# Kernel tuning notes

Hardware: AMD Instinct MI355X
Metric: run time of the kernel (lower is better)

The kernel has to match this reference:

```python
import jax, jax.numpy as jnp
import numpy as np

B, S, D_MODEL = 2, 2048, 1024
NUM_HEADS, ATTN_DIM = 16, 64


def setup_inputs() -> dict:
    key = jax.random.key(0)
    ks = jax.random.split(key, 9)
    scale = 1.0 / np.sqrt(D_MODEL)
    states = jax.random.normal(ks[0], (B, S, D_MODEL), dtype=jnp.float32)
    Wq = jax.random.normal(ks[1], (D_MODEL, NUM_HEADS * ATTN_DIM), dtype=jnp.float32) * scale
    bq = jnp.zeros((NUM_HEADS * ATTN_DIM,), dtype=jnp.float32)
    Wk = jax.random.normal(ks[2], (D_MODEL, NUM_HEADS * ATTN_DIM), dtype=jnp.float32) * scale
    bk = jnp.zeros((NUM_HEADS * ATTN_DIM,), dtype=jnp.float32)
    Wv = jax.random.normal(ks[3], (D_MODEL, NUM_HEADS * ATTN_DIM), dtype=jnp.float32) * scale
    bv = jnp.zeros((NUM_HEADS * ATTN_DIM,), dtype=jnp.float32)
    Wo = jax.random.normal(ks[4], (NUM_HEADS * ATTN_DIM, D_MODEL), dtype=jnp.float32) * scale
    bo = jnp.zeros((D_MODEL,), dtype=jnp.float32)
    return {"states": states, "Wq": Wq, "bq": bq, "Wk": Wk, "bk": bk,
            "Wv": Wv, "bv": bv, "Wo": Wo, "bo": bo}


def reference(states, Wq, bq, Wk, bk, Wv, bv, Wo, bo):
    b, s, _ = states.shape
    h, d = NUM_HEADS, ATTN_DIM

    def proj(W, bias):
        # tanh-activated Dense, then split heads: [b, s, h*d] -> [b, h, s, d]
        y = jnp.tanh(states @ W + bias)
        return y.reshape(b, s, h, d).transpose(0, 2, 1, 3)

    q, k, v = proj(Wq, bq), proj(Wk, bk), proj(Wv, bv)
    # scores: [b, h, s, s]
    alpha = jnp.einsum("bhqd,bhkd->bhqk", q, k) / jnp.sqrt(jnp.float32(d))
    # causal mask (row i attends to cols 0..i); masked logits set to float32.min
    causal = jnp.tril(jnp.ones((s, s), dtype=bool))
    alpha = jnp.where(causal, alpha, jnp.finfo(jnp.float32).min)
    alpha = jax.nn.softmax(alpha, axis=-1)
    ctx = jnp.einsum("bhqk,bhkd->bhqd", alpha, v)  # [b, h, s, d]
    ctx = ctx.transpose(0, 2, 1, 3).reshape(b, s, h * d)
    return jnp.tanh(ctx @ Wo + bo)
```

## Files before the change

### kernel.cpp

```cpp
#include <hip/hip_runtime.h>
#include <math.h>

typedef unsigned short u16;
typedef __attribute__((ext_vector_type(4))) float f32x4;
typedef __attribute__((ext_vector_type(16))) float f32x16;
typedef __attribute__((ext_vector_type(8))) short bf16x8;

#define B_ 2
#define S_ 2048
#define DM 1024
#define H_ 16
#define AD 64
#define ME 4194304
#define SC 0.18033688011112042f
#define SMAX 12.0f

#define GLL(g, s) __builtin_amdgcn_global_load_lds( \
  (const __attribute__((address_space(1))) void*)(g), \
  (__attribute__((address_space(3))) void*)(s), 16, 0, 0)

__device__ inline u16 f2bf(float f) {
  union { float f; unsigned u; } v; v.f = f;
  unsigned r = v.u + 0x7fffu + ((v.u >> 16) & 1u);
  return (u16)(r >> 16);
}

__device__ inline unsigned cvt_pk_bf16(float lo, float hi) {
  unsigned r;
  asm("v_cvt_pk_bf16_f32 %0, %1, %2" : "=v"(r) : "v"(lo), "v"(hi));
  return r;
}

__device__ inline float fast_tanh(float x) {
  float e = __builtin_amdgcn_exp2f(x * 2.885390081777927f);
  return 1.f - 2.f * __builtin_amdgcn_rcpf(e + 1.f);
}

__global__ __launch_bounds__(256) void conv_states(const float* __restrict__ in,
                                                   u16* __restrict__ out) {
  int i = (blockIdx.x * 256 + threadIdx.x) * 8;
  const float4* p = (const float4*)(in + i);
  float4 a = p[0], b = p[1];
  bf16x8 o;
  o[0] = (short)f2bf(a.x); o[1] = (short)f2bf(a.y);
  o[2] = (short)f2bf(a.z); o[3] = (short)f2bf(a.w);
  o[4] = (short)f2bf(b.x); o[5] = (short)f2bf(b.y);
  o[6] = (short)f2bf(b.z); o[7] = (short)f2bf(b.w);
  *(bf16x8*)&out[i] = o;
}

__global__ void transpose_w(const float* __restrict__ Wq, const float* __restrict__ Wk,
                            const float* __restrict__ Wv, const float* __restrict__ Wo,
                            u16* __restrict__ Wt) {
  __shared__ float t[32][33];
  int z = blockIdx.z;
  const float* W = (z == 0) ? Wq : (z == 1) ? Wk : (z == 2) ? Wv : Wo;
  u16* out = Wt + (size_t)z * DM * DM;
  int n0 = blockIdx.x * 32, k0 = blockIdx.y * 32;
  int tx = threadIdx.x, ty = threadIdx.y;
  t[ty][tx] = W[(k0 + ty) * DM + n0 + tx];
  __syncthreads();
  out[(n0 + ty) * DM + k0 + tx] = f2bf(t[tx][ty]);
}

__global__ __launch_bounds__(256) void qkv_gemm(
    const u16* __restrict__ A, const u16* __restrict__ Wt,
    const float* __restrict__ bq, const float* __restrict__ bk, const float* __restrict__ bv,
    u16* __restrict__ Qw, u16* __restrict__ Kw, u16* __restrict__ Vtw) {
  __shared__ __attribute__((aligned(16))) u16 lA[128 * 32];
  __shared__ __attribute__((aligned(16))) u16 lB[128 * 32];
  const int z = blockIdx.z;
  const u16* Bt = Wt + (size_t)z * DM * DM;
  const int lin = blockIdx.y * 8 + blockIdx.x;
  const int tile = (lin & 7) * 32 + (lin >> 3);
  const int m0 = (tile >> 3) * 128, n0 = (tile & 7) * 128;
  const int tid = threadIdx.x;
  const int wid = tid >> 6, l = tid & 63;
  const int lr = l & 15, lk = l >> 4;
  const int wm = (wid >> 1) * 64, wn = (wid & 1) * 64;
  const int srow = wid * 32 + (l >> 2);
  const int scol = (l & 3) * 8;

  f32x4 acc[4][4] = {};

  for (int k0 = 0; k0 < DM; k0 += 32) {
    const u16* gA = &A[(size_t)(m0 + srow) * DM + k0 + scol];
    const u16* gB = &Bt[(size_t)(n0 + srow) * DM + k0 + scol];
    GLL(gA,           lA + wid * 1024);
    GLL(gA + 16 * DM, lA + wid * 1024 + 512);
    GLL(gB,           lB + wid * 1024);
    GLL(gB + 16 * DM, lB + wid * 1024 + 512);
    __syncthreads();
    bf16x8 af[4], bfr[4];
#pragma unroll
    for (int g = 0; g < 4; ++g) {
      af[g]  = *(const bf16x8*)&lA[(wm + g * 16 + lr) * 32 + lk * 8];
      bfr[g] = *(const bf16x8*)&lB[(wn + g * 16 + lr) * 32 + lk * 8];
    }
#pragma unroll
    for (int mg = 0; mg < 4; ++mg)
#pragma unroll
      for (int ng = 0; ng < 4; ++ng)
        acc[mg][ng] = __builtin_amdgcn_mfma_f32_16x16x32_bf16(af[mg], bfr[ng], acc[mg][ng], 0, 0, 0);
    __syncthreads();
  }

  const float* bias = (z == 0) ? bq : (z == 1) ? bk : bv;
#pragma unroll
  for (int mg = 0; mg < 4; ++mg)
#pragma unroll
    for (int ng = 0; ng < 4; ++ng)
#pragma unroll
      for (int r = 0; r < 4; ++r) {
        int m = m0 + wm + mg * 16 + lk * 4 + r;
        int n = n0 + wn + ng * 16 + lr;
        float v = fast_tanh(acc[mg][ng][r] + bias[n]);
        if (z == 0) v *= SC;
        u16 h16 = f2bf(v);
        int bb = m >> 11, s = m & 2047, hh = n >> 6, d = n & 63;
        if (z == 2) Vtw[((size_t)(bb * H_ + hh) * AD + d) * S_ + s] = h16;
        else ((z == 0) ? Qw : Kw)[((size_t)(bb * H_ + hh) * S_ + s) * AD + d] = h16;
      }
}

__global__ __launch_bounds__(256) void out_gemm(
    const u16* __restrict__ A, const u16* __restrict__ Bt,
    const float* __restrict__ bo, float* __restrict__ out) {
  __shared__ __attribute__((aligned(16))) u16 lA[128 * 32];
  __shared__ __attribute__((aligned(16))) u16 lB[128 * 32];
  const int lin = blockIdx.y * 8 + blockIdx.x;
  const int tile = (lin & 7) * 32 + (lin >> 3);
  const int m0 = (tile >> 3) * 128, n0 = (tile & 7) * 128;
  const int tid = threadIdx.x;
  const int wid = tid >> 6, l = tid & 63;
  const int lr = l & 15, lk = l >> 4;
  const int wm = (wid >> 1) * 64, wn = (wid & 1) * 64;
  const int srow = wid * 32 + (l >> 2);
  const int scol = (l & 3) * 8;

  f32x4 acc[4][4] = {};

  for (int k0 = 0; k0 < DM; k0 += 32) {
    const u16* gA = &A[(size_t)(m0 + srow) * DM + k0 + scol];
    const u16* gB = &Bt[(size_t)(n0 + srow) * DM + k0 + scol];
    GLL(gA,           lA + wid * 1024);
    GLL(gA + 16 * DM, lA + wid * 1024 + 512);
    GLL(gB,           lB + wid * 1024);
    GLL(gB + 16 * DM, lB + wid * 1024 + 512);
    __syncthreads();
    bf16x8 af[4], bfr[4];
#pragma unroll
    for (int g = 0; g < 4; ++g) {
      af[g]  = *(const bf16x8*)&lA[(wm + g * 16 + lr) * 32 + lk * 8];
      bfr[g] = *(const bf16x8*)&lB[(wn + g * 16 + lr) * 32 + lk * 8];
    }
#pragma unroll
    for (int mg = 0; mg < 4; ++mg)
#pragma unroll
      for (int ng = 0; ng < 4; ++ng)
        acc[mg][ng] = __builtin_amdgcn_mfma_f32_16x16x32_bf16(af[mg], bfr[ng], acc[mg][ng], 0, 0, 0);
    __syncthreads();
  }

#pragma unroll
  for (int mg = 0; mg < 4; ++mg)
#pragma unroll
    for (int ng = 0; ng < 4; ++ng)
#pragma unroll
      for (int r = 0; r < 4; ++r) {
        int m = m0 + wm + mg * 16 + lk * 4 + r;
        int n = n0 + wn + ng * 16 + lr;
        out[(size_t)m * DM + n] = fast_tanh(acc[mg][ng][r] + bo[n]);
      }
}

__global__ __launch_bounds__(256, 3) void attn_kernel(
    const u16* __restrict__ Q, const u16* __restrict__ K,
    const u16* __restrict__ Vt, u16* __restrict__ ctx,
    float* __restrict__ O0, float* __restrict__ O1, float* __restrict__ O2,
    float* __restrict__ L0, float* __restrict__ L1, float* __restrict__ L2) {
  __shared__ __attribute__((aligned(16))) char smem[32768];
  const int u = blockIdx.x >> 5;
  const int bh = blockIdx.x & 31;
  int t, lo;
  if (u < 11)       { t = u + 5;  lo = 0; }
  else if (u < 16)  { t = u;      lo = 6; }
  else if (u == 16) { t = 4;      lo = 0; }
  else if (u == 17) { t = 10;     lo = 6; }
  else { int r = u - 18, g = r / 3, c = r % 3;
         if (c == 0)      { t = 3 - g;  lo = 0; }
         else if (c == 1) { t = 9 - g;  lo = 6; }
         else             { t = 15 - g; lo = 12; } }
  const int hi = (lo == 0) ? (t < 5 ? t : 5) : ((lo == 6) ? (t < 11 ? t : 11) : t);

  const int tid = threadIdx.x, wl = tid >> 6, l = tid & 63;
  const int lq = l & 31, hl = l >> 5;
  const int q0 = t * 128 + wl * 32;

  const char* Qb = (const char*)(Q + (size_t)bh * S_ * AD);
  const char* Kb = (const char*)(K + (size_t)bh * S_ * AD);
  const char* Vb = (const char*)(Vt + (size_t)bh * AD * S_);

  int kcst[4], vcst[4], ldso[4];
#pragma unroll
  for (int i = 0; i < 4; ++i) {
    int c = wl * 4 + i;
    int o = c * 1024 + l * 16;
    ldso[i] = c * 1024 + l * 16;
    int row = o >> 8;
    int un = (o & 255) ^ ((row & 15) << 4);
    kcst[i] = (row * 2 + (un >> 7)) * 128 + (un & 127);
    vcst[i] = row * (2 * S_) + un;
  }

  bf16x8 qf[4];
#pragma unroll
  for (int ds = 0; ds < 4; ++ds)
    qf[ds] = *(const bf16x8*)(Qb + (size_t)(q0 + lq) * 128 + ds * 32 + hl * 16);

  f32x16 accO[2] = {};
  float lsum = 0.f;

  {
    bf16x8 kr[4], vr[4];
#pragma unroll
    for (int i = 0; i < 4; ++i) {
      kr[i] = *(const bf16x8*)(Kb + (size_t)lo * 16384 + kcst[i]);
      vr[i] = *(const bf16x8*)(Vb + (size_t)lo * 256  + vcst[i]);
    }
#pragma unroll
    for (int i = 0; i < 4; ++i) {
      *(bf16x8*)(smem + ldso[i])         = kr[i];
      *(bf16x8*)(smem + 16384 + ldso[i]) = vr[i];
    }
  }
  __syncthreads();

  const char* kl = smem;
  const char* vl = smem + 16384;

  auto sblock = [&](int s, bool tri) {
    f32x16 c = {};
    const int kvl = s * 32 + lq;
    const int rp = kvl >> 1, kbit = kvl & 1;
    const int swz = (rp & 15) << 4;
    __builtin_amdgcn_s_setprio(1);
#pragma unroll
    for (int ds = 0; ds < 4; ++ds) {
      bf16x8 a = *(const bf16x8*)(kl + rp * 256 +
                   (((kbit << 7) | (ds * 32 + hl * 16)) ^ swz));
      c = __builtin_amdgcn_mfma_f32_32x32x16_bf16(a, qf[ds], c, 0, 0, 0);
    }
    __builtin_amdgcn_s_setprio(0);

#pragma unroll
    for (int r = 0; r < 16; ++r) {
      float e = __builtin_amdgcn_exp2f(c[r] - SMAX);
      if (tri) {
        int kc = (r & 3) + 8 * (r >> 2) + 4 * hl;
        if (kc > lq) e = 0.f;
      }
      c[r] = e;
      lsum += e;
    }

    unsigned uu[8];
#pragma unroll
    for (int i = 0; i < 8; ++i)
      uu[i] = cvt_pk_bf16(c[2 * i], c[2 * i + 1]);
    unsigned s0a = uu[0], s0b = uu[2];
    unsigned s1a = uu[1], s1b = uu[3];
    unsigned s2a = uu[4], s2b = uu[6];
    unsigned s3a = uu[5], s3b = uu[7];
    asm("v_permlane32_swap_b32 %0, %1" : "+v"(s0a), "+v"(s0b));
    asm("v_permlane32_swap_b32 %0, %1" : "+v"(s1a), "+v"(s1b));
    asm("v_permlane32_swap_b32 %0, %1" : "+v"(s2a), "+v"(s2b));
    asm("v_permlane32_swap_b32 %0, %1" : "+v"(s3a), "+v"(s3b));
    union { unsigned w[4]; bf16x8 v; } c0_, c1_;
    c0_.w[0] = s0a; c0_.w[1] = s1a; c0_.w[2] = s0b; c0_.w[3] = s1b;
    c1_.w[0] = s2a; c1_.w[1] = s3a; c1_.w[2] = s2b; c1_.w[3] = s3b;

    __builtin_amdgcn_s_setprio(1);
#pragma unroll
    for (int d = 0; d < 2; ++d) {
      const int drow = d * 32 + lq;
      const int vswz = (drow & 15) << 4;
      bf16x8 a0 = *(const bf16x8*)(vl + drow * 256 + ((s * 64 + hl * 16) ^ vswz));
      bf16x8 a1 = *(const bf16x8*)(vl + drow * 256 + ((s * 64 + 32 + hl * 16) ^ vswz));
      accO[d] = __builtin_amdgcn_mfma_f32_32x32x16_bf16(a0, c0_.v, accO[d], 0, 0, 0);
      accO[d] = __builtin_amdgcn_mfma_f32_32x32x16_bf16(a1, c1_.v, accO[d], 0, 0, 0);
    }
    __builtin_amdgcn_s_setprio(0);
  };

  for (int kb = lo; kb <= hi; ++kb) {
    bf16x8 krn[4], vrn[4];
    const bool pf = (kb < hi);
    if (pf) {
#pragma unroll
      for (int i = 0; i < 4; ++i) {
        krn[i] = *(const bf16x8*)(Kb + (size_t)(kb + 1) * 16384 + kcst[i]);
        vrn[i] = *(const bf16x8*)(Vb + (size_t)(kb + 1) * 256  + vcst[i]);
      }
    }

    if (kb != t) {
#pragma unroll
      for (int s = 0; s < 4; ++s) sblock(s, false);
    } else {
      for (int s = 0; s < wl; ++s) sblock(s, false);
      sblock(wl, true);
    }

    __syncthreads();
    if (pf) {
#pragma unroll
      for (int i = 0; i < 4; ++i) {
        *(bf16x8*)(smem + ldso[i])         = krn[i];
        *(bf16x8*)(smem + 16384 + ldso[i]) = vrn[i];
      }
    }
    __syncthreads();
  }

  lsum += __shfl_xor(lsum, 32);
  const int q = q0 + lq;

  if (lo == 0 && t < 6) {
    const float inv = 1.f / lsum;
    u16* cb_ = ctx + ((size_t)(bh >> 4) * S_ + q) * DM + (bh & 15) * AD;
#pragma unroll
    for (int d = 0; d < 2; ++d)
#pragma unroll
      for (int g = 0; g < 4; ++g) {
        unsigned w0 = cvt_pk_bf16(accO[d][4 * g] * inv,     accO[d][4 * g + 1] * inv);
        unsigned w1 = cvt_pk_bf16(accO[d][4 * g + 2] * inv, accO[d][4 * g + 3] * inv);
        unsigned* dst = (unsigned*)(cb_ + d * 32 + 8 * g + 4 * hl);
        dst[0] = w0; dst[1] = w1;
      }
  } else {
    float* Ob; float* Lb;
    if (lo == 0)      { size_t r = (size_t)bh * 1280 + (q - 768);  Ob = O0 + r * 64; Lb = L0 + r; }
    else if (lo == 6) { size_t r = (size_t)bh * 1280 + (q - 768);  Ob = O1 + r * 64; Lb = L1 + r; }
    else              { size_t r = (size_t)bh * 512  + (q - 1536); Ob = O2 + r * 64; Lb = L2 + r; }
#pragma unroll
    for (int d = 0; d < 2; ++d)
#pragma unroll
      for (int g = 0; g < 4; ++g) {
        f32x4 w;
        w[0] = accO[d][4 * g];     w[1] = accO[d][4 * g + 1];
        w[2] = accO[d][4 * g + 2]; w[3] = accO[d][4 * g + 3];
        *(f32x4*)&Ob[d * 32 + 8 * g + 4 * hl] = w;
      }
    if (!hl) *Lb = lsum;
  }
}

__global__ __launch_bounds__(256) void attn_norm(
    const float* __restrict__ O0, const float* __restrict__ O1,
    const float* __restrict__ O2, const float* __restrict__ L0,
    const float* __restrict__ L1, const float* __restrict__ L2,
    u16* __restrict__ ctx) {
  const int tid = threadIdx.x;
  const int rowl = blockIdx.x * 64 + (tid >> 2);
  const int sub = tid & 3;
  const int bh = rowl / 1280, qr = rowl - bh * 1280;
  const int q = 768 + qr;
  float lv = L0[rowl] + L1[rowl];
  const f32x4* p0 = (const f32x4*)(O0 + (size_t)rowl * 64 + sub * 16);
  const f32x4* p1 = (const f32x4*)(O1 + (size_t)rowl * 64 + sub * 16);
  f32x4 v0 = p0[0] + p1[0], v1 = p0[1] + p1[1];
  f32x4 v2 = p0[2] + p1[2], v3 = p0[3] + p1[3];
  if (q >= 1536) {
    size_t r2 = (size_t)bh * 512 + (q - 1536);
    lv += L2[r2];
    const f32x4* p2 = (const f32x4*)(O2 + r2 * 64 + sub * 16);
    v0 += p2[0]; v1 += p2[1]; v2 += p2[2]; v3 += p2[3];
  }
  const float inv = 1.f / lv;
  const int b = bh >> 4, h = bh & 15;
  unsigned w[8];
  w[0] = cvt_pk_bf16(v0[0] * inv, v0[1] * inv);
  w[1] = cvt_pk_bf16(v0[2] * inv, v0[3] * inv);
  w[2] = cvt_pk_bf16(v1[0] * inv, v1[1] * inv);
  w[3] = cvt_pk_bf16(v1[2] * inv, v1[3] * inv);
  w[4] = cvt_pk_bf16(v2[0] * inv, v2[1] * inv);
  w[5] = cvt_pk_bf16(v2[2] * inv, v2[3] * inv);
  w[6] = cvt_pk_bf16(v3[0] * inv, v3[1] * inv);
  w[7] = cvt_pk_bf16(v3[2] * inv, v3[3] * inv);
  unsigned* dst = (unsigned*)(ctx + ((size_t)b * S_ + q) * DM + h * AD + sub * 16);
#pragma unroll
  for (int i = 0; i < 8; ++i) dst[i] = w[i];
}

extern "C" void kernel_launch(void* const* d_in, const int* in_sizes, int n_in,
                              void* d_out, int out_size, void* d_ws, size_t ws_size,
                              hipStream_t stream) {
  const float* states = (const float*)d_in[0];
  const float* Wq = (const float*)d_in[1];
  const float* bq = (const float*)d_in[2];
  const float* Wk = (const float*)d_in[3];
  const float* bk = (const float*)d_in[4];
  const float* Wv = (const float*)d_in[5];
  const float* bv = (const float*)d_in[6];
  const float* Wo = (const float*)d_in[7];
  const float* bo = (const float*)d_in[8];
  float* out = (float*)d_out;

  u16* sbf = (u16*)d_ws;
  u16* wt  = sbf + ME;
  u16* Qw  = wt + ME;
  u16* Kw  = Qw + ME;
  u16* Vtw = Kw + ME;
  u16* ctx = Vtw + ME;
  float* O0 = (float*)(ctx + ME);
  float* O1 = O0 + (size_t)32 * 1280 * 64;
  float* O2 = (float*)d_ws;
  float* L0 = O2 + (size_t)32 * 512 * 64;
  float* L1 = L0 + 32 * 1280;
  float* L2 = L1 + 32 * 1280;

  conv_states<<<ME / (256 * 8), 256, 0, stream>>>(states, sbf);
  transpose_w<<<dim3(32, 32, 4), dim3(32, 32), 0, stream>>>(Wq, Wk, Wv, Wo, wt);
  qkv_gemm<<<dim3(8, 32, 3), 256, 0, stream>>>(sbf, wt, bq, bk, bv, Qw, Kw, Vtw);
  attn_kernel<<<960, 256, 0, stream>>>(Qw, Kw, Vtw, ctx, O0, O1, O2, L0, L1, L2);
  attn_norm<<<640, 256, 0, stream>>>(O0, O1, O2, L0, L1, L2, ctx);
  out_gemm<<<dim3(8, 32), 256, 0, stream>>>(ctx, wt + 3 * (size_t)DM * DM, bo, out);
}
```

Baseline: 121.3 us.

## Fuse split-KV combine into attention via atomic counters; merge prep kernels

Merges the states conversion and weight transpose into a single prep launch, which also zeroes a counter array. The separate attn_norm kernel is removed. Each split-KV attention block now increments a per-tile atomic counter, and the last arriving chunk sums the partial O/L buffers, normalizes, and writes the bf16 ctx rows. This removes two launches and a kernel boundary, at the cost of threadfences, an atomic per block, and serialized combine work in the last-finishing block.

```diff
diff --git a/kernel.cpp b/kernel.cpp
--- a/kernel.cpp
+++ b/kernel.cpp
@@ -36,31 +36,30 @@
   return 1.f - 2.f * __builtin_amdgcn_rcpf(e + 1.f);
 }
 
-__global__ __launch_bounds__(256) void conv_states(const float* __restrict__ in,
-                                                   u16* __restrict__ out) {
-  int i = (blockIdx.x * 256 + threadIdx.x) * 8;
-  const float4* p = (const float4*)(in + i);
-  float4 a = p[0], b = p[1];
-  bf16x8 o;
-  o[0] = (short)f2bf(a.x); o[1] = (short)f2bf(a.y);
-  o[2] = (short)f2bf(a.z); o[3] = (short)f2bf(a.w);
-  o[4] = (short)f2bf(b.x); o[5] = (short)f2bf(b.y);
-  o[6] = (short)f2bf(b.z); o[7] = (short)f2bf(b.w);
-  *(bf16x8*)&out[i] = o;
-}
-
-__global__ void transpose_w(const float* __restrict__ Wq, const float* __restrict__ Wk,
-                            const float* __restrict__ Wv, const float* __restrict__ Wo,
-                            u16* __restrict__ Wt) {
+__global__ void prep(const float* __restrict__ Wq, const float* __restrict__ Wk,
+                     const float* __restrict__ Wv, const float* __restrict__ Wo,
+                     u16* __restrict__ Wt, const float* __restrict__ states,
+                     u16* __restrict__ sbf, int* __restrict__ cnt) {
   __shared__ float t[32][33];
-  int z = blockIdx.z;
-  const float* W = (z == 0) ? Wq : (z == 1) ? Wk : (z == 2) ? Wv : Wo;
-  u16* out = Wt + (size_t)z * DM * DM;
-  int n0 = blockIdx.x * 32, k0 = blockIdx.y * 32;
-  int tx = threadIdx.x, ty = threadIdx.y;
-  t[ty][tx] = W[(k0 + ty) * DM + n0 + tx];
-  __syncthreads();
-  out[(n0 + ty) * DM + k0 + tx] = f2bf(t[tx][ty]);
+  const int z = blockIdx.z;
+  const int tx = threadIdx.x, ty = threadIdx.y;
+  if (z < 4) {
+    const float* W = (z == 0) ? Wq : (z == 1) ? Wk : (z == 2) ? Wv : Wo;
+    u16* out = Wt + (size_t)z * DM * DM;
+    int n0 = blockIdx.x * 32, k0 = blockIdx.y * 32;
+    t[ty][tx] = W[(k0 + ty) * DM + n0 + tx];
+    __syncthreads();
+    out[(n0 + ty) * DM + k0 + tx] = f2bf(t[tx][ty]);
+  } else {
+    const int lin = blockIdx.y * 32 + blockIdx.x;
+    const int tl = ty * 32 + tx;
+    const int i = (lin * 1024 + tl) * 4;
+    float4 a = *(const float4*)(states + i);
+    ushort4 o;
+    o.x = f2bf(a.x); o.y = f2bf(a.y); o.z = f2bf(a.z); o.w = f2bf(a.w);
+    *(ushort4*)&sbf[i] = o;
+    if (lin == 0 && tl < 512) cnt[tl] = 0;
+  }
 }
 
 __global__ __launch_bounds__(256) void qkv_gemm(
@@ -178,8 +177,10 @@
     const u16* __restrict__ Q, const u16* __restrict__ K,
     const u16* __restrict__ Vt, u16* __restrict__ ctx,
     float* __restrict__ O0, float* __restrict__ O1, float* __restrict__ O2,
-    float* __restrict__ L0, float* __restrict__ L1, float* __restrict__ L2) {
+    float* __restrict__ L0, float* __restrict__ L1, float* __restrict__ L2,
+    int* __restrict__ cnt) {
   __shared__ __attribute__((aligned(16))) char smem[32768];
+  __shared__ int lastf;
   const int u = blockIdx.x >> 5;
   const int bh = blockIdx.x & 31;
   int t, lo;
@@ -353,44 +354,43 @@
         *(f32x4*)&Ob[d * 32 + 8 * g + 4 * hl] = w;
       }
     if (!hl) *Lb = lsum;
-  }
-}
-
-__global__ __launch_bounds__(256) void attn_norm(
-    const float* __restrict__ O0, const float* __restrict__ O1,
-    const float* __restrict__ O2, const float* __restrict__ L0,
-    const float* __restrict__ L1, const float* __restrict__ L2,
-    u16* __restrict__ ctx) {
-  const int tid = threadIdx.x;
-  const int rowl = blockIdx.x * 64 + (tid >> 2);
-  const int sub = tid & 3;
-  const int bh = rowl / 1280, qr = rowl - bh * 1280;
-  const int q = 768 + qr;
-  float lv = L0[rowl] + L1[rowl];
-  const f32x4* p0 = (const f32x4*)(O0 + (size_t)rowl * 64 + sub * 16);
-  const f32x4* p1 = (const f32x4*)(O1 + (size_t)rowl * 64 + sub * 16);
-  f32x4 v0 = p0[0] + p1[0], v1 = p0[1] + p1[1];
-  f32x4 v2 = p0[2] + p1[2], v3 = p0[3] + p1[3];
-  if (q >= 1536) {
-    size_t r2 = (size_t)bh * 512 + (q - 1536);
-    lv += L2[r2];
-    const f32x4* p2 = (const f32x4*)(O2 + r2 * 64 + sub * 16);
-    v0 += p2[0]; v1 += p2[1]; v2 += p2[2]; v3 += p2[3];
-  }
-  const float inv = 1.f / lv;
-  const int b = bh >> 4, h = bh & 15;
-  unsigned w[8];
-  w[0] = cvt_pk_bf16(v0[0] * inv, v0[1] * inv);
-  w[1] = cvt_pk_bf16(v0[2] * inv, v0[3] * inv);
-  w[2] = cvt_pk_bf16(v1[0] * inv, v1[1] * inv);
-  w[3] = cvt_pk_bf16(v1[2] * inv, v1[3] * inv);
-  w[4] = cvt_pk_bf16(v2[0] * inv, v2[1] * inv);
-  w[5] = cvt_pk_bf16(v2[2] * inv, v2[3] * inv);
-  w[6] = cvt_pk_bf16(v3[0] * inv, v3[1] * inv);
-  w[7] = cvt_pk_bf16(v3[2] * inv, v3[3] * inv);
-  unsigned* dst = (unsigned*)(ctx + ((size_t)b * S_ + q) * DM + h * AD + sub * 16);
-#pragma unroll
-  for (int i = 0; i < 8; ++i) dst[i] = w[i];
+
+    __threadfence();
+    __syncthreads();
+    const int nch = (t >= 12) ? 3 : 2;
+    if (tid == 0) {
+      int old = atomicAdd(&cnt[bh * 16 + t], 1);
+      lastf = (old == nch - 1);
+    }
+    __syncthreads();
+    if (lastf) {
+      __threadfence();
+      const int rq = t * 128 + (tid >> 1);
+      const size_t r01 = (size_t)bh * 1280 + (rq - 768);
+      float lv = L0[r01] + L1[r01];
+      const f32x4* s0 = (const f32x4*)(O0 + r01 * 64 + (tid & 1) * 32);
+      const f32x4* s1 = (const f32x4*)(O1 + r01 * 64 + (tid & 1) * 32);
+      f32x4 v[8];
+#pragma unroll
+      for (int i = 0; i < 8; ++i) v[i] = s0[i] + s1[i];
+      if (t >= 12) {
+        const size_t r2 = (size_t)bh * 512 + (rq - 1536);
+        lv += L2[r2];
+        const f32x4* s2 = (const f32x4*)(O2 + r2 * 64 + (tid & 1) * 32);
+#pragma unroll
+        for (int i = 0; i < 8; ++i) v[i] += s2[i];
+      }
+      const float inv = 1.f / lv;
+      unsigned* dst = (unsigned*)(ctx + ((size_t)(bh >> 4) * S_ + rq) * DM +
+                                  (bh & 15) * AD + (tid & 1) * 32);
+#pragma unroll
+      for (int i = 0; i < 8; ++i) {
+        dst[2 * i]     = cvt_pk_bf16(v[i][0] * inv, v[i][1] * inv);
+        dst[2 * i + 1] = cvt_pk_bf16(v[i][2] * inv, v[i][3] * inv);
+      }
+      if (tid == 0) cnt[bh * 16 + t] = 0;
+    }
+  }
 }
 
 extern "C" void kernel_launch(void* const* d_in, const int* in_sizes, int n_in,
@@ -415,15 +415,14 @@
   u16* ctx = Vtw + ME;
   float* O0 = (float*)(ctx + ME);
   float* O1 = O0 + (size_t)32 * 1280 * 64;
+  int*  cnt = (int*)(O1 + (size_t)32 * 1280 * 64);
   float* O2 = (float*)d_ws;
   float* L0 = O2 + (size_t)32 * 512 * 64;
   float* L1 = L0 + 32 * 1280;
   float* L2 = L1 + 32 * 1280;
 
-  conv_states<<<ME / (256 * 8), 256, 0, stream>>>(states, sbf);
-  transpose_w<<<dim3(32, 32, 4), dim3(32, 32), 0, stream>>>(Wq, Wk, Wv, Wo, wt);
+  prep<<<dim3(32, 32, 5), dim3(32, 32), 0, stream>>>(Wq, Wk, Wv, Wo, wt, states, sbf, cnt);
   qkv_gemm<<<dim3(8, 32, 3), 256, 0, stream>>>(sbf, wt, bq, bk, bv, Qw, Kw, Vtw);
-  attn_kernel<<<960, 256, 0, stream>>>(Qw, Kw, Vtw, ctx, O0, O1, O2, L0, L1, L2);
-  attn_norm<<<640, 256, 0, stream>>>(O0, O1, O2, L0, L1, L2, ctx);
+  attn_kernel<<<960, 256, 0, stream>>>(Qw, Kw, Vtw, ctx, O0, O1, O2, L0, L1, L2, cnt);
   out_gemm<<<dim3(8, 32), 256, 0, stream>>>(ctx, wt + 3 * (size_t)DM * DM, bo, out);
 }
```

After: 278.5 us. +129.6%, slower.
